# Optimization experiments

Hardware: AMD Instinct MI355X
Metric: run time of the kernel (lower is better)

## Reference

```python
import jax, jax.numpy as jnp
import numpy as np

D_MODEL = 2048
N_HEADS = 16
KV_HEADS = 4
HEAD_DIM = D_MODEL // N_HEADS  # 128
B, T = 2, 2048


def setup_inputs() -> dict:
    key = jax.random.key(0)
    ks = jax.random.split(key, 8)
    s = 1.0 / np.sqrt(D_MODEL)
    x = jax.random.normal(ks[0], (B, T, D_MODEL), dtype=jnp.float32)
    # Linear weights stored as (in_features, out_features); y = x @ W
    Wq = jax.random.normal(ks[1], (D_MODEL, D_MODEL), dtype=jnp.float32) * s
    Wk = jax.random.normal(ks[2], (D_MODEL, KV_HEADS * HEAD_DIM), dtype=jnp.float32) * s
    Wv = jax.random.normal(ks[3], (D_MODEL, KV_HEADS * HEAD_DIM), dtype=jnp.float32) * s
    Wo = jax.random.normal(ks[4], (D_MODEL, D_MODEL), dtype=jnp.float32) * s
    weight_logits = jnp.ones((KV_HEADS,), dtype=jnp.float32)
    weight_values = jnp.ones((KV_HEADS,), dtype=jnp.float32)
    # additive causal mask (1, 1, T, T): 0 on/below diag, -inf above
    neg_inf = jnp.float32(-1e30)
    causal = jnp.tril(jnp.ones((T, T), dtype=bool))
    attn_mask = jnp.where(causal, jnp.float32(0.0), neg_inf)[None, None]
    return {"x": x, "attn_mask": attn_mask, "Wq": Wq, "Wk": Wk, "Wv": Wv,
            "Wo": Wo, "weight_logits": weight_logits, "weight_values": weight_values}


def reference(x, attn_mask, Wq, Wk, Wv, Wo, weight_logits, weight_values):
    Bx, Tx, _ = x.shape
    H, G, D = N_HEADS, KV_HEADS, HEAD_DIM
    group_size = H // G
    head_to_group = jnp.arange(H) // group_size  # (H,)

    q = (x @ Wq).reshape(Bx, Tx, H, D).transpose(0, 2, 1, 3)  # (B,H,T,D)
    k = (x @ Wk).reshape(Bx, Tx, G, D).transpose(0, 2, 1, 3)  # (B,G,T,D)
    v = (x @ Wv).reshape(Bx, Tx, G, D).transpose(0, 2, 1, 3)  # (B,G,T,D)

    # GQA expansion: gather kv groups per head
    k_g = k[:, head_to_group]  # (B,H,T,D)
    v_g = v[:, head_to_group]  # (B,H,T,D)
    # (use_value_weight=False: weight_values unused)

    logit_scale = weight_logits[head_to_group][None, :, None, None]  # (1,H,1,1)
    inv_sqrt_d = jnp.float32(1.0 / np.sqrt(D))
    logits = jnp.einsum('bhqd,bhkd->bhqk', q, k_g) * inv_sqrt_d * logit_scale
    logits = logits + attn_mask
    attn = jax.nn.softmax(logits, axis=-1)  # dropout p=0 -> identity
    y = jnp.einsum('bhqk,bhkd->bhqd', attn, v_g)
    y = y.transpose(0, 2, 1, 3).reshape(Bx, Tx, H * D)
    return y @ Wo
```

## Files before the change

kernel.cpp:

```cpp
#include <hip/hip_runtime.h>
#include <hip/hip_bf16.h>

#define TT 2048
#define DM 2048
#define NH 16
#define KVH 4
#define HD 128

typedef __attribute__((ext_vector_type(8))) short bs8;
typedef __attribute__((ext_vector_type(4))) float fx4;
typedef __attribute__((ext_vector_type(4))) unsigned short us4;
typedef __attribute__((ext_vector_type(8))) unsigned short us8;

#if __has_builtin(__builtin_amdgcn_exp2f)
#define EXP2(x) __builtin_amdgcn_exp2f(x)
#else
#define EXP2(x) exp2f(x)
#endif

__device__ inline unsigned short f2b(float f) {
  __hip_bfloat16 h = __float2bfloat16(f);
  return *reinterpret_cast<unsigned short*>(&h);
}

__device__ inline float b2f(unsigned short u) {
  unsigned int v = ((unsigned int)u) << 16;
  return *reinterpret_cast<float*>(&v);
}

__device__ inline void gld_lds16(const ushort* g, ushort* l) {
  __builtin_amdgcn_global_load_lds(
      (const __attribute__((address_space(1))) void*)g,
      (__attribute__((address_space(3))) void*)l,
      16, 0, 0);
}

__global__ __launch_bounds__(256) void prep_kernel(
    const float* __restrict__ x, const float* __restrict__ Wq,
    const float* __restrict__ Wk, const float* __restrict__ Wv,
    const float* __restrict__ Wo, ushort* __restrict__ xb,
    ushort* __restrict__ Wqkvt, ushort* __restrict__ Wot) {
  int tx = threadIdx.x, ty = threadIdx.y;
  if (blockIdx.z == 2) {
    int lin = (blockIdx.y * 96 + blockIdx.x) * 256 + ty * 32 + tx;
#pragma unroll
    for (int it = 0; it < 2; ++it) {
      int i = lin + it * (6144 * 256);
      if (i < (TT * 2 * DM) / 4) {
        float4 v = ((const float4*)x)[i];
        us4 o = {f2b(v.x), f2b(v.y), f2b(v.z), f2b(v.w)};
        ((us4*)xb)[i] = o;
      }
    }
    return;
  }
  __shared__ float t[32][33];
  int n0 = blockIdx.x * 32, k0 = blockIdx.y * 32;
  if (blockIdx.z == 0) {
    const float* src;
    int srcN, col0;
    if (n0 < 2048) { src = Wq; srcN = 2048; col0 = n0; }
    else if (n0 < 2560) { src = Wk; srcN = 512; col0 = n0 - 2048; }
    else { src = Wv; srcN = 512; col0 = n0 - 2560; }
    for (int jj = 0; jj < 4; ++jj)
      t[ty + jj * 8][tx] = src[(size_t)(k0 + ty + jj * 8) * srcN + col0 + tx];
    __syncthreads();
    for (int jj = 0; jj < 4; ++jj)
      Wqkvt[(size_t)(n0 + ty + jj * 8) * 2048 + k0 + tx] = f2b(t[tx][ty + jj * 8]);
  } else {
    if (n0 >= 2048) return;
    for (int jj = 0; jj < 4; ++jj)
      t[ty + jj * 8][tx] = Wo[(size_t)(k0 + ty + jj * 8) * 2048 + n0 + tx];
    __syncthreads();
    for (int jj = 0; jj < 4; ++jj)
      Wot[(size_t)(n0 + ty + jj * 8) * 2048 + k0 + tx] = f2b(t[tx][ty + jj * 8]);
  }
}

#define EPI_STRIDE 136
__global__ __launch_bounds__(256) void gemm_qkv(const ushort* __restrict__ A,
                                                const ushort* __restrict__ Bt,
                                                ushort* __restrict__ qo,
                                                ushort* __restrict__ ko,
                                                ushort* __restrict__ vo,
                                                int K) {
  __shared__ alignas(16) ushort smem[128 * EPI_STRIDE];
  ushort* As = smem;
  ushort* Bs = smem + 8192;
  const int tid = threadIdx.x;
  const int lane = tid & 63;
  const int wid = tid >> 6;
  const int wm = wid >> 1, wn = wid & 1;
  const int quad = lane >> 4, l16 = lane & 15;
  const int bm = blockIdx.y * 128, bn = blockIdx.x * 128;

  fx4 acc[4][4];
  for (int i = 0; i < 4; ++i)
    for (int j = 0; j < 4; ++j) acc[i][j] = (fx4){0.f, 0.f, 0.f, 0.f};

  const int r8 = lane >> 3, s8 = lane & 7;
  for (int k0 = 0; k0 < K; k0 += 64) {
    for (int i = 0; i < 4; ++i) {
      int m = i * 32 + wid * 8 + r8;
      int c = s8 ^ (m & 7);
      gld_lds16(A + (size_t)(bm + m) * K + k0 + c * 8, As + (i * 32 + wid * 8) * 64);
      gld_lds16(Bt + (size_t)(bn + m) * K + k0 + c * 8, Bs + (i * 32 + wid * 8) * 64);
    }
    __syncthreads();
    for (int ks = 0; ks < 2; ++ks) {
      bs8 af[4], bf[4];
      for (int mt = 0; mt < 4; ++mt) {
        int m = wm * 64 + mt * 16 + l16;
        int c = ks * 4 + quad;
        int slot = c ^ (m & 7);
        af[mt] = *(const bs8*)(As + m * 64 + slot * 8);
      }
      for (int nt = 0; nt < 4; ++nt) {
        int n = wn * 64 + nt * 16 + l16;
        int c = ks * 4 + quad;
        int slot = c ^ (n & 7);
        bf[nt] = *(const bs8*)(Bs + n * 64 + slot * 8);
      }
      for (int mt = 0; mt < 4; ++mt)
        for (int nt = 0; nt < 4; ++nt)
          acc[mt][nt] = __builtin_amdgcn_mfma_f32_16x16x32_bf16(af[mt], bf[nt],
                                                                acc[mt][nt], 0, 0, 0);
    }
    __syncthreads();
  }

  for (int mt = 0; mt < 4; ++mt)
    for (int nt = 0; nt < 4; ++nt)
      for (int r = 0; r < 4; ++r) {
        int row = wm * 64 + mt * 16 + quad * 4 + r;
        int col = wn * 64 + nt * 16 + l16;
        smem[row * EPI_STRIDE + col] = f2b(acc[mt][nt][r]);
      }
  __syncthreads();
  const int rsel = tid >> 4;
  const int csel = tid & 15;
  for (int ii = 0; ii < 8; ++ii) {
    int row = ii * 16 + rsel;
    us8 chunk = *(const us8*)(smem + row * EPI_STRIDE + csel * 8);
    int row_g = bm + row;
    int colc = bn + csel * 8;
    if (bn < 2048) {
      *(us8*)(qo + (size_t)row_g * 2048 + colc) = chunk;
    } else {
      int b = row_g >> 11, t = row_g & 2047;
      if (bn < 2560) {
        int kc = colc - 2048;
        int gg = kc >> 7, d = kc & 127;
        *(us8*)(ko + ((size_t)(b * KVH + gg) * TT + t) * HD + d) = chunk;
      } else {
        int vc = colc - 2560;
        int gg = vc >> 7, d = vc & 127;
        *(us8*)(vo + ((size_t)(b * KVH + gg) * TT + t) * HD + d) = chunk;
      }
    }
  }
}

__global__ __launch_bounds__(256) void transpose_v(const ushort* __restrict__ vin,
                                                   ushort* __restrict__ vout) {
  __shared__ ushort tl[32][33];
  int tx = threadIdx.x, ty = threadIdx.y;
  int t0 = blockIdx.x * 32, d0 = blockIdx.y * 32;
  size_t base = (size_t)blockIdx.z * TT * HD;
  for (int jj = 0; jj < 4; ++jj)
    tl[ty + jj * 8][tx] = vin[base + (size_t)(t0 + ty + jj * 8) * HD + d0 + tx];
  __syncthreads();
  for (int jj = 0; jj < 4; ++jj)
    vout[base + (size_t)(d0 + ty + jj * 8) * TT + t0 + tx] = tl[tx][ty + jj * 8];
}

__global__ __launch_bounds__(256) void gemm_out(const ushort* __restrict__ A,
                                                const ushort* __restrict__ Bt,
                                                float* __restrict__ Cout,
                                                int N, int K) {
  __shared__ alignas(16) ushort smem[128 * EPI_STRIDE];
  ushort* As = smem;
  ushort* Bs = smem + 8192;
  const int tid = threadIdx.x;
  const int lane = tid & 63;
  const int wid = tid >> 6;
  const int wm = wid >> 1, wn = wid & 1;
  const int quad = lane >> 4, l16 = lane & 15;
  const int bm = blockIdx.y * 128, bn = blockIdx.x * 128;

  fx4 acc[4][4];
  for (int i = 0; i < 4; ++i)
    for (int j = 0; j < 4; ++j) acc[i][j] = (fx4){0.f, 0.f, 0.f, 0.f};

  const int r8 = lane >> 3, s8 = lane & 7;
  for (int k0 = 0; k0 < K; k0 += 64) {
    for (int i = 0; i < 4; ++i) {
      int m = i * 32 + wid * 8 + r8;
      int c = s8 ^ (m & 7);
      gld_lds16(A + (size_t)(bm + m) * K + k0 + c * 8, As + (i * 32 + wid * 8) * 64);
      gld_lds16(Bt + (size_t)(bn + m) * K + k0 + c * 8, Bs + (i * 32 + wid * 8) * 64);
    }
    __syncthreads();
    for (int ks = 0; ks < 2; ++ks) {
      bs8 af[4], bf[4];
      for (int mt = 0; mt < 4; ++mt) {
        int m = wm * 64 + mt * 16 + l16;
        int c = ks * 4 + quad;
        int slot = c ^ (m & 7);
        af[mt] = *(const bs8*)(As + m * 64 + slot * 8);
      }
      for (int nt = 0; nt < 4; ++nt) {
        int n = wn * 64 + nt * 16 + l16;
        int c = ks * 4 + quad;
        int slot = c ^ (n & 7);
        bf[nt] = *(const bs8*)(Bs + n * 64 + slot * 8);
      }
      for (int mt = 0; mt < 4; ++mt)
        for (int nt = 0; nt < 4; ++nt)
          acc[mt][nt] = __builtin_amdgcn_mfma_f32_16x16x32_bf16(af[mt], bf[nt],
                                                                acc[mt][nt], 0, 0, 0);
    }
    __syncthreads();
  }

  for (int mt = 0; mt < 4; ++mt)
    for (int nt = 0; nt < 4; ++nt)
      for (int r = 0; r < 4; ++r) {
        int row = wm * 64 + mt * 16 + quad * 4 + r;
        int col = wn * 64 + nt * 16 + l16;
        smem[row * EPI_STRIDE + col] = f2b(acc[mt][nt][r]);
      }
  __syncthreads();
  const int rsel = tid >> 4;
  const int csel = tid & 15;
  for (int ii = 0; ii < 8; ++ii) {
    int row = ii * 16 + rsel;
    us8 chunk = *(const us8*)(smem + row * EPI_STRIDE + csel * 8);
    int row_g = bm + row;
    int colc = bn + csel * 8;
    float4 lo = {b2f(chunk[0]), b2f(chunk[1]), b2f(chunk[2]), b2f(chunk[3])};
    float4 hi = {b2f(chunk[4]), b2f(chunk[5]), b2f(chunk[6]), b2f(chunk[7])};
    *(float4*)(Cout + (size_t)row_g * N + colc) = lo;
    *(float4*)(Cout + (size_t)row_g * N + colc + 4) = hi;
  }
}

__global__ __launch_bounds__(256, 2) void attn_kernel(const ushort* __restrict__ qb,
                                                      const ushort* __restrict__ kb,
                                                      const ushort* __restrict__ vt,
                                                      ushort* __restrict__ yb,
                                                      const float* __restrict__ wlog) {
  __shared__ alignas(16) ushort Ks[2][64 * 128];
  __shared__ alignas(16) ushort Vs[2][128 * 64];
  __shared__ alignas(16) ushort Ps[128 * 64];

  const int bid = blockIdx.x;
  const int qt = (bid & 256) ? (bid & 15) : 15 - (bid & 15);
  const int h = (bid >> 4) & 15;
  const int b = bid >> 8;
  const int g = h >> 2;
  const int tid = threadIdx.x;
  const int lane = tid & 63;
  const int wid = tid >> 6;
  const int quad = lane >> 4;
  const int l16 = lane & 15;
  const int qwv = qt * 128 + wid * 32;

  const float scale = wlog[g] * 0.08838834764831845f;
  const float sc2 = scale * 1.4426950408889634f;

  const ushort* kbase = kb + (size_t)(b * KVH + g) * TT * HD;
  const ushort* vbase = vt + (size_t)(b * KVH + g) * HD * TT;

  const ushort* kp;
  const ushort* vp;
  {
    int keyr = wid * 4 + (lane >> 4);
    int si = lane & 15;
    int ck = (si & 8) | ((si ^ keyr) & 7);
    kp = kbase + (size_t)keyr * HD + ck * 8;
    int dr = wid * 8 + (lane >> 3);
    int s8 = lane & 7;
    int cv = s8 ^ (dr & 7);
    vp = vbase + (size_t)dr * TT + cv * 8;
  }

#pragma unroll
  for (int r = 0; r < 4; ++r) {
    gld_lds16(kp + (size_t)(16 * r) * HD, &Ks[0][r * 2048 + wid * 512]);
    gld_lds16(vp + (size_t)(32 * r) * TT, &Vs[0][r * 2048 + wid * 512]);
  }
  kp += 64 * HD;
  vp += 64;

  bs8 qf[2][4];
#pragma unroll
  for (int nt = 0; nt < 2; ++nt) {
    int q = qwv + nt * 16 + l16;
    const ushort* qrow = qb + ((size_t)(b * TT + q)) * DM + h * HD;
#pragma unroll
    for (int ks = 0; ks < 4; ++ks)
      qf[nt][ks] = *(const bs8*)(qrow + ks * 32 + quad * 8);
  }

  float m_i[2] = {-INFINITY, -INFINITY};
  float l_i[2] = {0.f, 0.f};
  fx4 o[8][2];
#pragma unroll
  for (int i = 0; i < 8; ++i)
#pragma unroll
    for (int nt = 0; nt < 2; ++nt) o[i][nt] = (fx4){0.f, 0.f, 0.f, 0.f};

  const int jmax = 2 * qt + 1;
  for (int j = 0; j <= jmax; ++j) {
    const int cur = j & 1;
    if (j < jmax) {
      const int nxt = cur ^ 1;
#pragma unroll
      for (int r = 0; r < 4; ++r) {
        gld_lds16(kp + (size_t)(16 * r) * HD, &Ks[nxt][r * 2048 + wid * 512]);
        gld_lds16(vp + (size_t)(32 * r) * TT, &Vs[nxt][r * 2048 + wid * 512]);
      }
      kp += 64 * HD;
      vp += 64;
      asm volatile("s_waitcnt vmcnt(8)" ::: "memory");
    } else {
      asm volatile("s_waitcnt vmcnt(0)" ::: "memory");
    }
    __builtin_amdgcn_s_barrier();

    if (j * 64 <= qwv + 31) {
      const ushort* Kc = Ks[cur];
      const ushort* Vc = Vs[cur];
      fx4 s[4][2];
#pragma unroll
      for (int mt = 0; mt < 4; ++mt)
#pragma unroll
        for (int nt = 0; nt < 2; ++nt) s[mt][nt] = (fx4){0.f, 0.f, 0.f, 0.f};
      __builtin_amdgcn_s_setprio(1);
#pragma unroll
      for (int mt = 0; mt < 4; ++mt) {
        int key = mt * 16 + l16;
#pragma unroll
        for (int ks = 0; ks < 4; ++ks) {
          int c = ks * 4 + quad;
          int slot = (c & 8) | ((c ^ key) & 7);
          bs8 a = *(const bs8*)(Kc + key * 128 + slot * 8);
          s[mt][0] = __builtin_amdgcn_mfma_f32_16x16x32_bf16(a, qf[0][ks],
                                                             s[mt][0], 0, 0, 0);
          s[mt][1] = __builtin_amdgcn_mfma_f32_16x16x32_bf16(a, qf[1][ks],
                                                             s[mt][1], 0, 0, 0);
        }
      }
      __builtin_amdgcn_s_setprio(0);

      if (j * 64 + 63 > qwv) {
#pragma unroll
        for (int nt = 0; nt < 2; ++nt) {
          int q = qwv + nt * 16 + l16;
#pragma unroll
          for (int mt = 0; mt < 4; ++mt)
#pragma unroll
            for (int r = 0; r < 4; ++r) {
              int key = j * 64 + mt * 16 + quad * 4 + r;
              if (key > q) s[mt][nt][r] = -1e30f;
            }
        }
      }
      float mx[2];
#pragma unroll
      for (int nt = 0; nt < 2; ++nt) {
        float m = s[0][nt][0];
#pragma unroll
        for (int mt = 0; mt < 4; ++mt)
#pragma unroll
          for (int r = 0; r < 4; ++r) m = fmaxf(m, s[mt][nt][r]);
        m = fmaxf(m, __shfl_xor(m, 16));
        m = fmaxf(m, __shfl_xor(m, 32));
        mx[nt] = m;
      }

      bool ok = ((mx[0] - m_i[0]) * scale <= 8.0f) &&
                ((mx[1] - m_i[1]) * scale <= 8.0f);
      if (!__all(ok)) {
#pragma unroll
        for (int nt = 0; nt < 2; ++nt) {
          float m_new = fmaxf(m_i[nt], mx[nt]);
          float alpha = EXP2((m_i[nt] - m_new) * sc2);
          l_i[nt] *= alpha;
#pragma unroll
          for (int dmt = 0; dmt < 8; ++dmt)
#pragma unroll
            for (int r = 0; r < 4; ++r) o[dmt][nt][r] *= alpha;
          m_i[nt] = m_new;
        }
      }
#pragma unroll
      for (int nt = 0; nt < 2; ++nt) {
        float negb = -m_i[nt] * sc2;
        float sum = 0.f;
#pragma unroll
        for (int mt = 0; mt < 4; ++mt)
#pragma unroll
          for (int r = 0; r < 4; ++r) {
            float pv = EXP2(fmaf(s[mt][nt][r], sc2, negb));
            s[mt][nt][r] = pv;
            sum += pv;
          }
        sum += __shfl_xor(sum, 16);
        sum += __shfl_xor(sum, 32);
        l_i[nt] += sum;
      }

      const int sw = l16 & 7;
#pragma unroll
      for (int nt = 0; nt < 2; ++nt) {
        int qrow = wid * 32 + nt * 16 + l16;
#pragma unroll
        for (int mt = 0; mt < 4; ++mt) {
          us4 pw = {f2b(s[mt][nt][0]), f2b(s[mt][nt][1]),
                    f2b(s[mt][nt][2]), f2b(s[mt][nt][3])};
          int chunk = mt * 2 + (quad >> 1);
          *(us4*)(Ps + qrow * 64 + ((chunk ^ sw) << 3) + ((quad & 1) << 2)) = pw;
        }
      }

#pragma unroll
      for (int ks = 0; ks < 2; ++ks) {
        int qrow0 = wid * 32 + l16;
        bs8 pb0 = *(const bs8*)(Ps + qrow0 * 64 + (((ks * 4 + quad) ^ sw) << 3));
        bs8 pb1 = *(const bs8*)(Ps + (qrow0 + 16) * 64 + (((ks * 4 + quad) ^ sw) << 3));
        __builtin_amdgcn_s_setprio(1);
#pragma unroll
        for (int dmt = 0; dmt < 8; ++dmt) {
          int d = dmt * 16 + l16;
          int c = ks * 4 + quad;
          int slot = c ^ (d & 7);
          bs8 va = *(const bs8*)(Vc + d * 64 + slot * 8);
          o[dmt][0] = __builtin_amdgcn_mfma_f32_16x16x32_bf16(va, pb0, o[dmt][0], 0, 0, 0);
          o[dmt][1] = __builtin_amdgcn_mfma_f32_16x16x32_bf16(va, pb1, o[dmt][1], 0, 0, 0);
        }
        __builtin_amdgcn_s_setprio(0);
      }
    }
    asm volatile("s_waitcnt lgkmcnt(0)" ::: "memory");
    __builtin_amdgcn_s_barrier();
  }

#pragma unroll
  for (int nt = 0; nt < 2; ++nt) {
    float inv = 1.0f / l_i[nt];
    int q = qwv + nt * 16 + l16;
    ushort* yrow = yb + ((size_t)(b * TT + q)) * DM + h * HD;
#pragma unroll
    for (int dmt = 0; dmt < 8; ++dmt) {
      us4 w = {f2b(o[dmt][nt][0] * inv), f2b(o[dmt][nt][1] * inv),
               f2b(o[dmt][nt][2] * inv), f2b(o[dmt][nt][3] * inv)};
      *(us4*)(yrow + dmt * 16 + quad * 4) = w;
    }
  }
}

extern "C" void kernel_launch(void* const* d_in, const int* in_sizes, int n_in,
                              void* d_out, int out_size, void* d_ws, size_t ws_size,
                              hipStream_t stream) {
  const float* x = (const float*)d_in[0];
  const float* Wq = (const float*)d_in[2];
  const float* Wk = (const float*)d_in[3];
  const float* Wv = (const float*)d_in[4];
  const float* Wo = (const float*)d_in[5];
  const float* wlog = (const float*)d_in[6];

  char* ws = (char*)d_ws;
  ushort* xb = (ushort*)ws;     ws += (size_t)4096 * 2048 * 2;
  ushort* Wqkvt = (ushort*)ws;  ws += (size_t)3072 * 2048 * 2;
  ushort* Wot = (ushort*)ws;    ws += (size_t)2048 * 2048 * 2;
  ushort* qbuf = (ushort*)ws;   ws += (size_t)4096 * 2048 * 2;
  ushort* kbuf = (ushort*)ws;   ws += (size_t)2 * KVH * 2048 * 128 * 2;
  ushort* vtmp = (ushort*)ws;   ws += (size_t)2 * KVH * 2048 * 128 * 2;
  ushort* vbuf = (ushort*)ws;   ws += (size_t)2 * KVH * 2048 * 128 * 2;
  ushort* ybuf = (ushort*)ws;   ws += (size_t)4096 * 2048 * 2;

  prep_kernel<<<dim3(96, 64, 3), dim3(32, 8), 0, stream>>>(
      x, Wq, Wk, Wv, Wo, xb, Wqkvt, Wot);
  gemm_qkv<<<dim3(24, 32), 256, 0, stream>>>(xb, Wqkvt, qbuf, kbuf, vtmp, 2048);
  transpose_v<<<dim3(64, 4, 8), dim3(32, 8), 0, stream>>>(vtmp, vbuf);
  attn_kernel<<<512, 256, 0, stream>>>(qbuf, kbuf, vbuf, ybuf, wlog);
  gemm_out<<<dim3(16, 32), 256, 0, stream>>>(ybuf, Wot, (float*)d_out, 2048, 2048);
}
```

Before: 305.1 us.

## Split attention key tiles across wave pairs with LDS softmax merge

The attention block grows to 512 threads (8 waves). Each pair of waves shares one 32-row query slice and splits each 64-key tile into two halves, each wave keeping its own online-softmax state. At the end the two partial outputs are merged through shared memory using the max/sum rescaling. Fetching K tile fragments is also batched ahead of the MFMAs. The aim is more waves in flight to hide latency and more parallelism per block, at the cost of a merge step, a final sync, and more register and LDS pressure at occupancy 4.

```diff
diff --git a/kernel.cpp b/kernel.cpp
--- a/kernel.cpp
+++ b/kernel.cpp
@@ -245,14 +245,15 @@
   }
 }
 
-__global__ __launch_bounds__(256, 2) void attn_kernel(const ushort* __restrict__ qb,
+__global__ __launch_bounds__(512, 4) void attn_kernel(const ushort* __restrict__ qb,
                                                       const ushort* __restrict__ kb,
                                                       const ushort* __restrict__ vt,
                                                       ushort* __restrict__ yb,
                                                       const float* __restrict__ wlog) {
-  __shared__ alignas(16) ushort Ks[2][64 * 128];
-  __shared__ alignas(16) ushort Vs[2][128 * 64];
-  __shared__ alignas(16) ushort Ps[128 * 64];
+  __shared__ alignas(16) ushort smem[40960];
+  ushort* KsBuf = smem;
+  ushort* VsBuf = smem + 16384;
+  ushort* Ps = smem + 32768;
 
   const int bid = blockIdx.x;
   const int qt = (bid & 256) ? (bid & 15) : 15 - (bid & 15);
@@ -262,9 +263,11 @@
   const int tid = threadIdx.x;
   const int lane = tid & 63;
   const int wid = tid >> 6;
+  const int qg = wid >> 1;
+  const int kh = wid & 1;
   const int quad = lane >> 4;
   const int l16 = lane & 15;
-  const int qwv = qt * 128 + wid * 32;
+  const int qwv = qt * 128 + qg * 32;
 
   const float scale = wlog[g] * 0.08838834764831845f;
   const float sc2 = scale * 1.4426950408889634f;
@@ -285,11 +288,10 @@
     vp = vbase + (size_t)dr * TT + cv * 8;
   }
 
-#pragma unroll
-  for (int r = 0; r < 4; ++r) {
-    gld_lds16(kp + (size_t)(16 * r) * HD, &Ks[0][r * 2048 + wid * 512]);
-    gld_lds16(vp + (size_t)(32 * r) * TT, &Vs[0][r * 2048 + wid * 512]);
-  }
+  gld_lds16(kp, KsBuf + wid * 512);
+  gld_lds16(kp + 32 * HD, KsBuf + 4096 + wid * 512);
+  gld_lds16(vp, VsBuf + wid * 512);
+  gld_lds16(vp + 64 * TT, VsBuf + 4096 + wid * 512);
   kp += 64 * HD;
   vp += 64;
 
@@ -316,53 +318,56 @@
     const int cur = j & 1;
     if (j < jmax) {
       const int nxt = cur ^ 1;
-#pragma unroll
-      for (int r = 0; r < 4; ++r) {
-        gld_lds16(kp + (size_t)(16 * r) * HD, &Ks[nxt][r * 2048 + wid * 512]);
-        gld_lds16(vp + (size_t)(32 * r) * TT, &Vs[nxt][r * 2048 + wid * 512]);
-      }
+      gld_lds16(kp, KsBuf + nxt * 8192 + wid * 512);
+      gld_lds16(kp + 32 * HD, KsBuf + nxt * 8192 + 4096 + wid * 512);
+      gld_lds16(vp, VsBuf + nxt * 8192 + wid * 512);
+      gld_lds16(vp + 64 * TT, VsBuf + nxt * 8192 + 4096 + wid * 512);
       kp += 64 * HD;
       vp += 64;
-      asm volatile("s_waitcnt vmcnt(8)" ::: "memory");
+      asm volatile("s_waitcnt vmcnt(4)" ::: "memory");
     } else {
       asm volatile("s_waitcnt vmcnt(0)" ::: "memory");
     }
     __builtin_amdgcn_s_barrier();
 
-    if (j * 64 <= qwv + 31) {
-      const ushort* Kc = Ks[cur];
-      const ushort* Vc = Vs[cur];
-      fx4 s[4][2];
-#pragma unroll
-      for (int mt = 0; mt < 4; ++mt)
+    if (j * 64 + kh * 32 <= qwv + 31) {
+      const ushort* Kc = KsBuf + cur * 8192;
+      const ushort* Vc = VsBuf + cur * 8192;
+      fx4 s[2][2];
+#pragma unroll
+      for (int mt = 0; mt < 2; ++mt)
 #pragma unroll
         for (int nt = 0; nt < 2; ++nt) s[mt][nt] = (fx4){0.f, 0.f, 0.f, 0.f};
       __builtin_amdgcn_s_setprio(1);
 #pragma unroll
-      for (int mt = 0; mt < 4; ++mt) {
-        int key = mt * 16 + l16;
+      for (int mt = 0; mt < 2; ++mt) {
+        int key = kh * 32 + mt * 16 + l16;
+        bs8 a[4];
 #pragma unroll
         for (int ks = 0; ks < 4; ++ks) {
           int c = ks * 4 + quad;
           int slot = (c & 8) | ((c ^ key) & 7);
-          bs8 a = *(const bs8*)(Kc + key * 128 + slot * 8);
-          s[mt][0] = __builtin_amdgcn_mfma_f32_16x16x32_bf16(a, qf[0][ks],
+          a[ks] = *(const bs8*)(Kc + key * 128 + slot * 8);
+        }
+#pragma unroll
+        for (int ks = 0; ks < 4; ++ks) {
+          s[mt][0] = __builtin_amdgcn_mfma_f32_16x16x32_bf16(a[ks], qf[0][ks],
                                                              s[mt][0], 0, 0, 0);
-          s[mt][1] = __builtin_amdgcn_mfma_f32_16x16x32_bf16(a, qf[1][ks],
+          s[mt][1] = __builtin_amdgcn_mfma_f32_16x16x32_bf16(a[ks], qf[1][ks],
                                                              s[mt][1], 0, 0, 0);
         }
       }
       __builtin_amdgcn_s_setprio(0);
 
-      if (j * 64 + 63 > qwv) {
+      if (j * 64 + kh * 32 + 31 > qwv) {
 #pragma unroll
         for (int nt = 0; nt < 2; ++nt) {
           int q = qwv + nt * 16 + l16;
 #pragma unroll
-          for (int mt = 0; mt < 4; ++mt)
+          for (int mt = 0; mt < 2; ++mt)
 #pragma unroll
             for (int r = 0; r < 4; ++r) {
-              int key = j * 64 + mt * 16 + quad * 4 + r;
+              int key = j * 64 + kh * 32 + mt * 16 + quad * 4 + r;
               if (key > q) s[mt][nt][r] = -1e30f;
             }
         }
@@ -372,7 +377,7 @@
       for (int nt = 0; nt < 2; ++nt) {
         float m = s[0][nt][0];
 #pragma unroll
-        for (int mt = 0; mt < 4; ++mt)
+        for (int mt = 0; mt < 2; ++mt)
 #pragma unroll
           for (int r = 0; r < 4; ++r) m = fmaxf(m, s[mt][nt][r]);
         m = fmaxf(m, __shfl_xor(m, 16));
@@ -400,7 +405,7 @@
         float negb = -m_i[nt] * sc2;
         float sum = 0.f;
 #pragma unroll
-        for (int mt = 0; mt < 4; ++mt)
+        for (int mt = 0; mt < 2; ++mt)
 #pragma unroll
           for (int r = 0; r < 4; ++r) {
             float pv = EXP2(fmaf(s[mt][nt][r], sc2, negb));
@@ -415,26 +420,25 @@
       const int sw = l16 & 7;
 #pragma unroll
       for (int nt = 0; nt < 2; ++nt) {
-        int qrow = wid * 32 + nt * 16 + l16;
-#pragma unroll
-        for (int mt = 0; mt < 4; ++mt) {
+        int qrow = qg * 32 + nt * 16 + l16;
+#pragma unroll
+        for (int mt = 0; mt < 2; ++mt) {
           us4 pw = {f2b(s[mt][nt][0]), f2b(s[mt][nt][1]),
                     f2b(s[mt][nt][2]), f2b(s[mt][nt][3])};
-          int chunk = mt * 2 + (quad >> 1);
+          int chunk = kh * 4 + mt * 2 + (quad >> 1);
           *(us4*)(Ps + qrow * 64 + ((chunk ^ sw) << 3) + ((quad & 1) << 2)) = pw;
         }
       }
 
-#pragma unroll
-      for (int ks = 0; ks < 2; ++ks) {
-        int qrow0 = wid * 32 + l16;
-        bs8 pb0 = *(const bs8*)(Ps + qrow0 * 64 + (((ks * 4 + quad) ^ sw) << 3));
-        bs8 pb1 = *(const bs8*)(Ps + (qrow0 + 16) * 64 + (((ks * 4 + quad) ^ sw) << 3));
+      {
+        int qrow0 = qg * 32 + l16;
+        int c = kh * 4 + quad;
+        bs8 pb0 = *(const bs8*)(Ps + qrow0 * 64 + ((c ^ sw) << 3));
+        bs8 pb1 = *(const bs8*)(Ps + (qrow0 + 16) * 64 + ((c ^ sw) << 3));
         __builtin_amdgcn_s_setprio(1);
 #pragma unroll
         for (int dmt = 0; dmt < 8; ++dmt) {
           int d = dmt * 16 + l16;
-          int c = ks * 4 + quad;
           int slot = c ^ (d & 7);
           bs8 va = *(const bs8*)(Vc + d * 64 + slot * 8);
           o[dmt][0] = __builtin_amdgcn_mfma_f32_16x16x32_bf16(va, pb0, o[dmt][0], 0, 0, 0);
@@ -447,16 +451,44 @@
     __builtin_amdgcn_s_barrier();
   }
 
-#pragma unroll
-  for (int nt = 0; nt < 2; ++nt) {
-    float inv = 1.0f / l_i[nt];
-    int q = qwv + nt * 16 + l16;
-    ushort* yrow = yb + ((size_t)(b * TT + q)) * DM + h * HD;
-#pragma unroll
-    for (int dmt = 0; dmt < 8; ++dmt) {
-      us4 w = {f2b(o[dmt][nt][0] * inv), f2b(o[dmt][nt][1] * inv),
-               f2b(o[dmt][nt][2] * inv), f2b(o[dmt][nt][3] * inv)};
-      *(us4*)(yrow + dmt * 16 + quad * 4) = w;
+  float* Ex = (float*)smem;
+  float* Ml = Ex + 4 * 32 * 132;
+  if (kh == 1) {
+#pragma unroll
+    for (int nt = 0; nt < 2; ++nt) {
+      float* exq = Ex + qg * 4224 + (nt * 16 + l16) * 132 + quad * 4;
+#pragma unroll
+      for (int dmt = 0; dmt < 8; ++dmt)
+        *(fx4*)(exq + dmt * 16) = o[dmt][nt];
+      if (quad == 0) {
+        Ml[qg * 64 + nt * 32 + l16] = m_i[nt];
+        Ml[qg * 64 + nt * 32 + 16 + l16] = l_i[nt];
+      }
+    }
+  }
+  __syncthreads();
+  if (kh == 0) {
+#pragma unroll
+    for (int nt = 0; nt < 2; ++nt) {
+      float m1 = Ml[qg * 64 + nt * 32 + l16];
+      float l1 = Ml[qg * 64 + nt * 32 + 16 + l16];
+      float m = fmaxf(m_i[nt], m1);
+      float a0 = EXP2((m_i[nt] - m) * sc2);
+      float a1 = EXP2((m1 - m) * sc2);
+      float inv = 1.0f / (l_i[nt] * a0 + l1 * a1);
+      float w0 = a0 * inv, w1 = a1 * inv;
+      int q = qwv + nt * 16 + l16;
+      ushort* yrow = yb + ((size_t)(b * TT + q)) * DM + h * HD;
+      const float* exq = Ex + qg * 4224 + (nt * 16 + l16) * 132 + quad * 4;
+#pragma unroll
+      for (int dmt = 0; dmt < 8; ++dmt) {
+        fx4 o1 = *(const fx4*)(exq + dmt * 16);
+        us4 w = {f2b(o[dmt][nt][0] * w0 + o1[0] * w1),
+                 f2b(o[dmt][nt][1] * w0 + o1[1] * w1),
+                 f2b(o[dmt][nt][2] * w0 + o1[2] * w1),
+                 f2b(o[dmt][nt][3] * w0 + o1[3] * w1)};
+        *(us4*)(yrow + dmt * 16 + quad * 4) = w;
+      }
     }
   }
 }
@@ -485,6 +517,6 @@
       x, Wq, Wk, Wv, Wo, xb, Wqkvt, Wot);
   gemm_qkv<<<dim3(24, 32), 256, 0, stream>>>(xb, Wqkvt, qbuf, kbuf, vtmp, 2048);
   transpose_v<<<dim3(64, 4, 8), dim3(32, 8), 0, stream>>>(vtmp, vbuf);
-  attn_kernel<<<512, 256, 0, stream>>>(qbuf, kbuf, vbuf, ybuf, wlog);
+  attn_kernel<<<512, 512, 0, stream>>>(qbuf, kbuf, vbuf, ybuf, wlog);
   gemm_out<<<dim3(16, 32), 256, 0, stream>>>(ybuf, Wot, (float*)d_out, 2048, 2048);
 }
```

Measured after the change: 426.0 us. 39.6% more time.
